# Kernel optimization log

Measured on AMD Instinct MI355X. Metric: run time of the kernel, lower is better.

Reference implementation:

```python
import jax, jax.numpy as jnp
import numpy as np

B, S, D = 8, 2048, 512
LN_EPS = 1e-5

def _layernorm(x, gamma, beta):
    mu = jnp.mean(x, axis=-1, keepdims=True)
    var = jnp.mean(jnp.square(x - mu), axis=-1, keepdims=True)
    return (x - mu) * jax.lax.rsqrt(var + LN_EPS) * gamma + beta

def setup_inputs() -> dict:
    key = jax.random.key(0)
    ks = jax.random.split(key, 10)
    s_in = 1.0 / np.sqrt(2 * D)
    s_d = 1.0 / np.sqrt(D)
    return {
        "Noise_x": jax.random.normal(ks[0], (B, S, D), jnp.float32),
        "X": jax.random.normal(ks[1], (B, S, D), jnp.float32),
        "cond": jax.random.normal(ks[2], (B, S, D), jnp.float32),
        "W_gate": jax.random.normal(ks[3], (2 * D, D), jnp.float32) * s_in,
        "b_gate": jnp.zeros((D,), jnp.float32),
        "W1": jax.random.normal(ks[4], (D, 2 * D), jnp.float32) * s_d,
        "b1": jnp.zeros((2 * D,), jnp.float32),
        "W2": jax.random.normal(ks[5], (2 * D, D), jnp.float32) * s_in,
        "b2": jnp.zeros((D,), jnp.float32),
        "g1": jnp.ones((D,), jnp.float32),
        "be1": jnp.zeros((D,), jnp.float32),
        "g2": jnp.ones((D,), jnp.float32),
        "be2": jnp.zeros((D,), jnp.float32),
    }

def reference(Noise_x, X, cond, W_gate, b_gate, W1, b1, W2, b2, g1, be1, g2, be2):
    # gated fusion of noise and condition
    combined = jnp.concatenate([Noise_x, cond], axis=-1)            # [B,S,2D]
    gate = jax.nn.sigmoid(combined @ W_gate + b_gate)               # [B,S,D]
    fused = gate * Noise_x + (1.0 - gate) * cond                    # [B,S,D]
    # hand-rolled attention: Q = fused, K = V = X
    scale = 1.0 / jnp.sqrt(jnp.asarray(D, fused.dtype))
    scores = jnp.einsum('bqd,bkd->bqk', fused, X) * scale           # [B,S,S]
    attn = jax.nn.softmax(scores, axis=-1)
    attn_out = jnp.einsum('bqk,bkd->bqd', attn, X)                  # [B,S,D]
    # residual + norm, FFN (exact GELU as in torch default), residual + norm
    q = _layernorm(fused + attn_out, g1, be1)
    ff = jax.nn.gelu(q @ W1 + b1, approximate=False) @ W2 + b2
    return _layernorm(q + ff, g2, be2)
```

## Files before the change

kernel.cpp:

```cpp
#include <hip/hip_runtime.h>
#include <math.h>

typedef unsigned short ushort_t;
typedef unsigned int uint_t;
typedef __attribute__((ext_vector_type(8))) short short8;
typedef __attribute__((ext_vector_type(4))) float floatx4;

constexpr int B = 8;
constexpr int S = 2048;
constexpr int D = 512;
constexpr int BS = B * S;
constexpr float LN_EPS = 1e-5f;
constexpr float ATTN_SCALE = 0.04419417382415922f;


__device__ __forceinline__ ushort_t f2bf(float f) {
    union { float f; uint_t u; } x; x.f = f;
    uint_t r = x.u + 0x7fffu + ((x.u >> 16) & 1u);
    return (ushort_t)(r >> 16);
}
__device__ __forceinline__ float bf2f(ushort_t h) {
    union { uint_t u; float f; } y; y.u = ((uint_t)h) << 16;
    return y.f;
}
__device__ __forceinline__ short8 pack8(float4 a, float4 b) {
    short8 p;
    p[0] = (short)f2bf(a.x); p[1] = (short)f2bf(a.y);
    p[2] = (short)f2bf(a.z); p[3] = (short)f2bf(a.w);
    p[4] = (short)f2bf(b.x); p[5] = (short)f2bf(b.y);
    p[6] = (short)f2bf(b.z); p[7] = (short)f2bf(b.w);
    return p;
}

#define SWZ_DECODE(bx, by, bz)                                                 \
    int bx, by, bz;                                                            \
    {                                                                          \
        const int gx = gridDim.x, gy = gridDim.y;                              \
        const int nwg = gx * gy * (int)gridDim.z;                              \
        const int F = blockIdx.x + gx * (blockIdx.y + gy * blockIdx.z);        \
        const int L = (F & 7) * (nwg >> 3) + (F >> 3);                         \
        bx = L % gx;                                                           \
        const int l2 = L / gx;                                                 \
        by = l2 % gy;                                                          \
        bz = l2 / gy;                                                          \
    }

__device__ __forceinline__ float blk_reduce_sum(float v, float* sm) {
#pragma unroll
    for (int o = 32; o; o >>= 1) v += __shfl_down(v, o, 64);
    __syncthreads();
    if ((threadIdx.x & 63) == 0) sm[threadIdx.x >> 6] = v;
    __syncthreads();
    return sm[0] + sm[1] + sm[2] + sm[3];
}
__device__ __forceinline__ float blk_reduce_max(float v, float* sm) {
#pragma unroll
    for (int o = 32; o; o >>= 1) v = fmaxf(v, __shfl_down(v, o, 64));
    __syncthreads();
    if ((threadIdx.x & 63) == 0) sm[threadIdx.x >> 6] = v;
    __syncthreads();
    return fmaxf(fmaxf(sm[0], sm[1]), fmaxf(sm[2], sm[3]));
}

__global__ __launch_bounds__(256) void transpose_cvt(
    const float* __restrict__ in, ushort_t* __restrict__ out, int R, int C,
    ushort_t* __restrict__ out2) {
    __shared__ float tl[32][33];
    const size_t zoff = (size_t)blockIdx.z * R * C;
    const int tx = threadIdx.x & 31, ty = threadIdx.x >> 5;
    const int c0 = blockIdx.x * 32, r0 = blockIdx.y * 32;
#pragma unroll
    for (int i = 0; i < 4; i++) {
        const float v = in[zoff + (size_t)(r0 + ty + i * 8) * C + c0 + tx];
        tl[ty + i * 8][tx] = v;
        if (out2) out2[zoff + (size_t)(r0 + ty + i * 8) * C + c0 + tx] = f2bf(v);
    }
    __syncthreads();
#pragma unroll
    for (int i = 0; i < 4; i++)
        out[zoff + (size_t)(c0 + ty + i * 8) * R + r0 + tx] = f2bf(tl[tx][ty + i * 8]);
}

#define IDX128()                                                               \
    const int t = threadIdx.x;                                                 \
    const int sr = t >> 2;                                          \
    const int sc = (t & 3) * 8;                                 \
    const int lane = t & 63, w = t >> 6;                                       \
    const int fr = lane & 15, fq = lane >> 4;

#define MFMA16(Asp, Bsp)                                                       \
    {                                                                          \
        short8 af[4], bfg[4];                                                  \
        _Pragma("unroll") for (int i = 0; i < 4; i++) {                        \
            af[i]  = *(const short8*)&(Asp)[(wm + i * 16 + fr) * 40 + fq * 8]; \
            bfg[i] = *(const short8*)&(Bsp)[(wn + i * 16 + fr) * 40 + fq * 8]; \
        }                                                                      \
        _Pragma("unroll") for (int i = 0; i < 4; i++)                          \
            _Pragma("unroll") for (int j = 0; j < 4; j++)                      \
                acc[i][j] = __builtin_amdgcn_mfma_f32_16x16x32_bf16(           \
                    af[i], bfg[j], acc[i][j], 0, 0, 0);                        \
    }

#define MFMA8(Asp, Bsp)                                                        \
    {                                                                          \
        short8 af[2], bfg[4];                                                  \
        _Pragma("unroll") for (int i = 0; i < 2; i++)                          \
            af[i]  = *(const short8*)&(Asp)[(wm + i * 16 + fr) * 40 + fq * 8]; \
        _Pragma("unroll") for (int j = 0; j < 4; j++)                          \
            bfg[j] = *(const short8*)&(Bsp)[(j * 16 + fr) * 40 + fq * 8];      \
        _Pragma("unroll") for (int i = 0; i < 2; i++)                          \
            _Pragma("unroll") for (int j = 0; j < 4; j++)                      \
                acc[i][j] = __builtin_amdgcn_mfma_f32_16x16x32_bf16(           \
                    af[i], bfg[j], acc[i][j], 0, 0, 0);                        \
    }

__global__ __launch_bounds__(256) void gate_gemm(
    const float* __restrict__ NX, const float* __restrict__ CD,
    const ushort_t* __restrict__ WgT, const float* __restrict__ bg,
    ushort_t* __restrict__ Fb) {
    __shared__ ushort_t As[2][128 * 40];
    __shared__ ushort_t Bs[2][128 * 40];
    SWZ_DECODE(bx, by, bz);
    (void)bz;
    IDX128();
    const int m0 = by * 128, n0 = bx * 128;
    const int wm = (w >> 1) * 64, wn = (w & 1) * 64;
    floatx4 acc[4][4];
#pragma unroll
    for (int i = 0; i < 4; i++)
#pragma unroll
        for (int j = 0; j < 4; j++) {
            acc[i][j][0] = 0.f; acc[i][j][1] = 0.f;
            acc[i][j][2] = 0.f; acc[i][j][3] = 0.f;
        }
    const ushort_t* Bb = WgT + (size_t)n0 * 1024;

    float4 f00, f01, f10, f11;
    int4 b0, b1;
    {
        const float* p0 = NX + (size_t)(m0 + sr) * 512 + sc;
        const float* p1 = NX + (size_t)(m0 + sr + 64) * 512 + sc;
        f00 = *(const float4*)p0;  f01 = *(const float4*)(p0 + 4);
        f10 = *(const float4*)p1;  f11 = *(const float4*)(p1 + 4);
        b0 = *(const int4*)(Bb + (size_t)sr * 1024 + sc);
        b1 = *(const int4*)(Bb + (size_t)(sr + 64) * 1024 + sc);
        *(short8*)&As[0][sr * 40 + sc] = pack8(f00, f01);
        *(short8*)&As[0][(sr + 64) * 40 + sc] = pack8(f10, f11);
        *(int4*)&Bs[0][sr * 40 + sc] = b0;
        *(int4*)&Bs[0][(sr + 64) * 40 + sc] = b1;
    }
    {
        const float* p0 = NX + (size_t)(m0 + sr) * 512 + 32 + sc;
        const float* p1 = NX + (size_t)(m0 + sr + 64) * 512 + 32 + sc;
        f00 = *(const float4*)p0;  f01 = *(const float4*)(p0 + 4);
        f10 = *(const float4*)p1;  f11 = *(const float4*)(p1 + 4);
        b0 = *(const int4*)(Bb + (size_t)sr * 1024 + 32 + sc);
        b1 = *(const int4*)(Bb + (size_t)(sr + 64) * 1024 + 32 + sc);
    }
    __syncthreads();

    int cur = 0;
    for (int k0 = 0; k0 < 1024; k0 += 32) {
        MFMA16(As[cur], Bs[cur]);
        const int kn = k0 + 32;
        if (kn < 1024) {
            *(short8*)&As[cur ^ 1][sr * 40 + sc] = pack8(f00, f01);
            *(short8*)&As[cur ^ 1][(sr + 64) * 40 + sc] = pack8(f10, f11);
            *(int4*)&Bs[cur ^ 1][sr * 40 + sc] = b0;
            *(int4*)&Bs[cur ^ 1][(sr + 64) * 40 + sc] = b1;
            const int kf = kn + 32;
            if (kf < 1024) {
                const float* Asrc = (kf < 512) ? NX : CD;
                const int kk = kf & 511;
                const float* p0 = Asrc + (size_t)(m0 + sr) * 512 + kk + sc;
                const float* p1 = Asrc + (size_t)(m0 + sr + 64) * 512 + kk + sc;
                f00 = *(const float4*)p0;  f01 = *(const float4*)(p0 + 4);
                f10 = *(const float4*)p1;  f11 = *(const float4*)(p1 + 4);
                b0 = *(const int4*)(Bb + (size_t)sr * 1024 + kf + sc);
                b1 = *(const int4*)(Bb + (size_t)(sr + 64) * 1024 + kf + sc);
            }
        }
        __syncthreads();
        cur ^= 1;
    }

#pragma unroll
    for (int i = 0; i < 4; i++) {
#pragma unroll
        for (int j = 0; j < 4; j++) {
#pragma unroll
            for (int r = 0; r < 4; r++) {
                const int m = m0 + wm + i * 16 + fq * 4 + r;
                const int n = n0 + wn + j * 16 + fr;
                const float z = acc[i][j][r] + bg[n];
                const float g = 1.f / (1.f + expf(-z));
                const size_t idx = (size_t)m * 512 + n;
                Fb[idx] = f2bf(g * NX[idx] + (1.f - g) * CD[idx]);
            }
        }
    }
}

template <int EPI>
__global__ __launch_bounds__(256) void gemm2_std(
    const ushort_t* __restrict__ A, int lda, long sAz,
    const ushort_t* __restrict__ Bt, int ldb, long sBz,
    void* __restrict__ Cv, int ldc, long sCz,
    int K, const float* __restrict__ bias, float scale, int init) {
    __shared__ ushort_t As[2][128 * 40];
    __shared__ ushort_t Bs[2][128 * 40];
    SWZ_DECODE(bx, by, bz);
    IDX128();
    const int m0 = by * 128, n0 = bx * 128;
    const int wm = (w >> 1) * 64, wn = (w & 1) * 64;
    floatx4 acc[4][4];
#pragma unroll
    for (int i = 0; i < 4; i++)
#pragma unroll
        for (int j = 0; j < 4; j++) {
            acc[i][j][0] = 0.f; acc[i][j][1] = 0.f;
            acc[i][j][2] = 0.f; acc[i][j][3] = 0.f;
        }
    const ushort_t* Ab = A + (size_t)bz * sAz + (size_t)m0 * lda;
    const ushort_t* Bb = Bt + (size_t)bz * sBz + (size_t)n0 * ldb;

    int4 a0 = *(const int4*)(Ab + (size_t)sr * lda + sc);
    int4 a1 = *(const int4*)(Ab + (size_t)(sr + 64) * lda + sc);
    int4 b0 = *(const int4*)(Bb + (size_t)sr * ldb + sc);
    int4 b1 = *(const int4*)(Bb + (size_t)(sr + 64) * ldb + sc);
    *(int4*)&As[0][sr * 40 + sc] = a0;
    *(int4*)&As[0][(sr + 64) * 40 + sc] = a1;
    *(int4*)&Bs[0][sr * 40 + sc] = b0;
    *(int4*)&Bs[0][(sr + 64) * 40 + sc] = b1;
    if (32 < K) {
        a0 = *(const int4*)(Ab + (size_t)sr * lda + 32 + sc);
        a1 = *(const int4*)(Ab + (size_t)(sr + 64) * lda + 32 + sc);
        b0 = *(const int4*)(Bb + (size_t)sr * ldb + 32 + sc);
        b1 = *(const int4*)(Bb + (size_t)(sr + 64) * ldb + 32 + sc);
    }
    __syncthreads();

    int cur = 0;
    for (int k0 = 0; k0 < K; k0 += 32) {
        MFMA16(As[cur], Bs[cur]);
        const int kn = k0 + 32;
        if (kn < K) {
            *(int4*)&As[cur ^ 1][sr * 40 + sc] = a0;
            *(int4*)&As[cur ^ 1][(sr + 64) * 40 + sc] = a1;
            *(int4*)&Bs[cur ^ 1][sr * 40 + sc] = b0;
            *(int4*)&Bs[cur ^ 1][(sr + 64) * 40 + sc] = b1;
            const int kf = kn + 32;
            if (kf < K) {
                a0 = *(const int4*)(Ab + (size_t)sr * lda + kf + sc);
                a1 = *(const int4*)(Ab + (size_t)(sr + 64) * lda + kf + sc);
                b0 = *(const int4*)(Bb + (size_t)sr * ldb + kf + sc);
                b1 = *(const int4*)(Bb + (size_t)(sr + 64) * ldb + kf + sc);
            }
        }
        __syncthreads();
        cur ^= 1;
    }

#pragma unroll
    for (int i = 0; i < 4; i++) {
#pragma unroll
        for (int j = 0; j < 4; j++) {
#pragma unroll
            for (int r = 0; r < 4; r++) {
                const int m = m0 + wm + i * 16 + fq * 4 + r;
                const int n = n0 + wn + j * 16 + fr;
                float v = acc[i][j][r];
                if (EPI == 0) {
                    ushort_t* C = (ushort_t*)Cv + (size_t)bz * sCz;
                    C[(size_t)m * ldc + n] = f2bf(v * scale);
                } else if (EPI == 1) {
                    const float x = v + bias[n];
                    const float gl = 0.5f * x * (1.f + erff(x * 0.70710678118654752f));
                    ushort_t* C = (ushort_t*)Cv;
                    C[(size_t)m * ldc + n] = f2bf(gl);
                } else {
                    float* T = (float*)Cv;
                    const size_t idx = (size_t)m * ldc + n;
                    T[idx] = T[idx] + v + (init ? bias[n] : 0.f);
                }
            }
        }
    }
}

template <int EPI>
__global__ __launch_bounds__(256) void gemm3_std(
    const ushort_t* __restrict__ A, int lda, long sAz,
    const ushort_t* __restrict__ Bt, int ldb, long sBz,
    void* __restrict__ Cv, int ldc, long sCz,
    int K, const float* __restrict__ bias, float scale, int init) {
    __shared__ ushort_t As[2][128 * 40];
    __shared__ ushort_t Bs[2][64 * 40];
    SWZ_DECODE(bx, by, bz);
    IDX128();
    const int m0 = by * 128, n0 = bx * 64;
    const int wm = w * 32;
    floatx4 acc[2][4];
#pragma unroll
    for (int i = 0; i < 2; i++)
#pragma unroll
        for (int j = 0; j < 4; j++) {
            acc[i][j][0] = 0.f; acc[i][j][1] = 0.f;
            acc[i][j][2] = 0.f; acc[i][j][3] = 0.f;
        }
    const ushort_t* Ab = A + (size_t)bz * sAz + (size_t)m0 * lda;
    const ushort_t* Bb = Bt + (size_t)bz * sBz + (size_t)n0 * ldb;

    int4 a0 = *(const int4*)(Ab + (size_t)sr * lda + sc);
    int4 a1 = *(const int4*)(Ab + (size_t)(sr + 64) * lda + sc);
    int4 b0 = *(const int4*)(Bb + (size_t)sr * ldb + sc);
    *(int4*)&As[0][sr * 40 + sc] = a0;
    *(int4*)&As[0][(sr + 64) * 40 + sc] = a1;
    *(int4*)&Bs[0][sr * 40 + sc] = b0;
    if (32 < K) {
        a0 = *(const int4*)(Ab + (size_t)sr * lda + 32 + sc);
        a1 = *(const int4*)(Ab + (size_t)(sr + 64) * lda + 32 + sc);
        b0 = *(const int4*)(Bb + (size_t)sr * ldb + 32 + sc);
    }
    __syncthreads();

    int cur = 0;
    for (int k0 = 0; k0 < K; k0 += 32) {
        MFMA8(As[cur], Bs[cur]);
        const int kn = k0 + 32;
        if (kn < K) {
            *(int4*)&As[cur ^ 1][sr * 40 + sc] = a0;
            *(int4*)&As[cur ^ 1][(sr + 64) * 40 + sc] = a1;
            *(int4*)&Bs[cur ^ 1][sr * 40 + sc] = b0;
            const int kf = kn + 32;
            if (kf < K) {
                a0 = *(const int4*)(Ab + (size_t)sr * lda + kf + sc);
                a1 = *(const int4*)(Ab + (size_t)(sr + 64) * lda + kf + sc);
                b0 = *(const int4*)(Bb + (size_t)sr * ldb + kf + sc);
            }
        }
        __syncthreads();
        cur ^= 1;
    }

#pragma unroll
    for (int i = 0; i < 2; i++) {
#pragma unroll
        for (int j = 0; j < 4; j++) {
#pragma unroll
            for (int r = 0; r < 4; r++) {
                const int m = m0 + wm + i * 16 + fq * 4 + r;
                const int n = n0 + j * 16 + fr;
                float v = acc[i][j][r];
                if (EPI == 0) {
                    ushort_t* C = (ushort_t*)Cv + (size_t)bz * sCz;
                    C[(size_t)m * ldc + n] = f2bf(v * scale);
                } else if (EPI == 1) {
                    const float x = v + bias[n];
                    const float gl = 0.5f * x * (1.f + erff(x * 0.70710678118654752f));
                    ushort_t* C = (ushort_t*)Cv;
                    C[(size_t)m * ldc + n] = f2bf(gl);
                } else {
                    float* T = (float*)Cv;
                    const size_t idx = (size_t)m * ldc + n;
                    T[idx] = T[idx] + v + (init ? bias[n] : 0.f);
                }
            }
        }
    }
}

__global__ __launch_bounds__(256) void softmax_bf16(ushort_t* __restrict__ Sc) {
    __shared__ float sm[4];
    ushort_t* row = Sc + (size_t)blockIdx.x * 2048;
    const int t = threadIdx.x;
    ushort_t raw[8];
    *(int4*)raw = *(const int4*)(row + t * 8);
    float e[8];
    float mx = -1e30f;
#pragma unroll
    for (int j = 0; j < 8; j++) { e[j] = bf2f(raw[j]); mx = fmaxf(mx, e[j]); }
    mx = blk_reduce_max(mx, sm);
    float s = 0.f;
#pragma unroll
    for (int j = 0; j < 8; j++) { e[j] = expf(e[j] - mx); s += e[j]; }
    s = blk_reduce_sum(s, sm);
    const float inv = 1.f / s;
#pragma unroll
    for (int j = 0; j < 8; j++) raw[j] = f2bf(e[j] * inv);
    *(int4*)(row + t * 8) = *(const int4*)raw;
}

__global__ __launch_bounds__(256) void ln1_kernel(
    const ushort_t* __restrict__ Fb, const ushort_t* __restrict__ Ab,
    const float* __restrict__ g1, const float* __restrict__ be1,
    float* __restrict__ qf, ushort_t* __restrict__ qb) {
    __shared__ float sm[4];
    const size_t base = (size_t)blockIdx.x * 512;
    const int t = threadIdx.x;
    const float v0 = bf2f(Fb[base + t]) + bf2f(Ab[base + t]);
    const float v1 = bf2f(Fb[base + t + 256]) + bf2f(Ab[base + t + 256]);
    const float mu = blk_reduce_sum(v0 + v1, sm) * (1.f / 512.f);
    const float d0 = v0 - mu, d1 = v1 - mu;
    const float var = blk_reduce_sum(d0 * d0 + d1 * d1, sm) * (1.f / 512.f);
    const float rs = rsqrtf(var + LN_EPS);
    const float y0 = d0 * rs * g1[t] + be1[t];
    const float y1 = d1 * rs * g1[t + 256] + be1[t + 256];
    qf[base + t] = y0;          qf[base + t + 256] = y1;
    qb[base + t] = f2bf(y0);    qb[base + t + 256] = f2bf(y1);
}

__global__ __launch_bounds__(256) void ln2_kernel(
    float* __restrict__ T, const float* __restrict__ g,
    const float* __restrict__ be) {
    __shared__ float sm[4];
    const size_t base = (size_t)blockIdx.x * 512;
    const int t = threadIdx.x;
    const float v0 = T[base + t];
    const float v1 = T[base + t + 256];
    const float mu = blk_reduce_sum(v0 + v1, sm) * (1.f / 512.f);
    const float d0 = v0 - mu, d1 = v1 - mu;
    const float var = blk_reduce_sum(d0 * d0 + d1 * d1, sm) * (1.f / 512.f);
    const float rs = rsqrtf(var + LN_EPS);
    T[base + t] = d0 * rs * g[t] + be[t];
    T[base + t + 256] = d1 * rs * g[t + 256] + be[t + 256];
}

extern "C" void kernel_launch(void* const* d_in, const int* in_sizes, int n_in,
                              void* d_out, int out_size, void* d_ws, size_t ws_size,
                              hipStream_t stream) {
    const float* NX  = (const float*)d_in[0];
    const float* X   = (const float*)d_in[1];
    const float* CD  = (const float*)d_in[2];
    const float* Wg  = (const float*)d_in[3];
    const float* bg  = (const float*)d_in[4];
    const float* W1  = (const float*)d_in[5];
    const float* b1  = (const float*)d_in[6];
    const float* W2  = (const float*)d_in[7];
    const float* b2  = (const float*)d_in[8];
    const float* g1  = (const float*)d_in[9];
    const float* be1 = (const float*)d_in[10];
    const float* g2  = (const float*)d_in[11];
    const float* be2 = (const float*)d_in[12];

    ushort_t* slot0 = (ushort_t*)d_ws;
    ushort_t* slot1 = (ushort_t*)((char*)d_ws + 16777216);
    ushort_t* slot2 = (ushort_t*)((char*)d_ws + 33554432);
    ushort_t* Xb    = slot0;
    ushort_t* attnb = slot0;
    ushort_t* hbuf  = slot0;
    ushort_t* Fb    = slot1;
    ushort_t* W1T   = slot1;
    ushort_t* W2T   = slot1 + 524288;
    ushort_t* WgT   = slot2;
    ushort_t* XbT   = slot2;
    ushort_t* qb    = slot2;
    ushort_t* Scb   = (ushort_t*)d_out;
    float*    qf    = (float*)d_out;

    transpose_cvt<<<dim3(512 / 32, 1024 / 32, 1), 256, 0, stream>>>(
        Wg, WgT, 1024, 512, nullptr);

    gate_gemm<<<dim3(4, 128), 256, 0, stream>>>(NX, CD, WgT, bg, Fb);

    transpose_cvt<<<dim3(512 / 32, 2048 / 32, 8), 256, 0, stream>>>(
        X, XbT, 2048, 512, Xb);

    for (int g = 0; g < 2; g++) {
        const size_t go = (size_t)g * 4 * S * 512;
        gemm2_std<0><<<dim3(16, 16, 4), 256, 0, stream>>>(
            Fb + go, D, (long)S * D,
            Xb + go, D, (long)S * D,
            (void*)Scb, S, (long)S * S, D, nullptr, ATTN_SCALE, 0);
        softmax_bf16<<<4 * S, 256, 0, stream>>>(Scb);
        gemm3_std<0><<<dim3(8, 16, 4), 256, 0, stream>>>(
            Scb, S, (long)S * S,
            XbT + go, S, (long)D * S,
            (void*)(attnb + go), 512, (long)S * 512, S, nullptr, 1.f, 0);
    }

    ln1_kernel<<<BS, 256, 0, stream>>>(Fb, attnb, g1, be1, qf, qb);

    transpose_cvt<<<dim3(1024 / 32, 512 / 32, 1), 256, 0, stream>>>(
        W1, W1T, 512, 1024, nullptr);
    transpose_cvt<<<dim3(512 / 32, 1024 / 32, 1), 256, 0, stream>>>(
        W2, W2T, 1024, 512, nullptr);

    for (int h = 0; h < 2; h++) {
        gemm2_std<1><<<dim3(4, 128), 256, 0, stream>>>(
            qb, 512, 0, W1T + (size_t)h * 512 * 512, 512, 0,
            (void*)hbuf, 512, 0, 512, b1 + h * 512, 1.f, 0);
        gemm2_std<2><<<dim3(4, 128), 256, 0, stream>>>(
            hbuf, 512, 0, W2T + h * 512, 1024, 0,
            (void*)qf, 512, 0, 512, b2, 1.f, h == 0 ? 1 : 0);
    }

    ln2_kernel<<<BS, 256, 0, stream>>>(qf, g2, be2);
}
```

Before: 513.5 us.

## Use 512-thread blocks with 8 waves for 128x128 GEMM tiles

The gate GEMM and the generic 128x128 GEMM kernels now run with 512 threads (8 waves) per block instead of 256. Each wave computes a 64x32 sub-tile instead of 64x64, which halves the accumulators and global-load registers per thread. Each thread now stages one A row and one B row per K step. The aim is more waves in flight to hide latency, at the cost of more LDS fragment reads per MFMA and heavier barrier synchronisation.

```diff
diff --git a/kernel.cpp b/kernel.cpp
--- a/kernel.cpp
+++ b/kernel.cpp
@@ -81,40 +81,28 @@
         out[zoff + (size_t)(c0 + ty + i * 8) * R + r0 + tx] = f2bf(tl[tx][ty + i * 8]);
 }
 
-#define IDX128()                                                               \
+#define IDX512()                                                               \
     const int t = threadIdx.x;                                                 \
-    const int sr = t >> 2;                                          \
-    const int sc = (t & 3) * 8;                                 \
-    const int lane = t & 63, w = t >> 6;                                       \
+    const int srow = t >> 2;                                       \
+    const int scol = (t & 3) * 8;                               \
+    const int lane = t & 63, w = t >> 6;                           \
+    const int wm = (w >> 2) * 64, wn = (w & 3) * 32;                           \
     const int fr = lane & 15, fq = lane >> 4;
 
-#define MFMA16(Asp, Bsp)                                                       \
+#define MFMA8W(Asp, Bsp)                                                       \
     {                                                                          \
-        short8 af[4], bfg[4];                                                  \
-        _Pragma("unroll") for (int i = 0; i < 4; i++) {                        \
+        short8 af[4], bfg[2];                                                  \
+        _Pragma("unroll") for (int i = 0; i < 4; i++)                          \
             af[i]  = *(const short8*)&(Asp)[(wm + i * 16 + fr) * 40 + fq * 8]; \
-            bfg[i] = *(const short8*)&(Bsp)[(wn + i * 16 + fr) * 40 + fq * 8]; \
-        }                                                                      \
+        _Pragma("unroll") for (int j = 0; j < 2; j++)                          \
+            bfg[j] = *(const short8*)&(Bsp)[(wn + j * 16 + fr) * 40 + fq * 8]; \
         _Pragma("unroll") for (int i = 0; i < 4; i++)                          \
-            _Pragma("unroll") for (int j = 0; j < 4; j++)                      \
+            _Pragma("unroll") for (int j = 0; j < 2; j++)                      \
                 acc[i][j] = __builtin_amdgcn_mfma_f32_16x16x32_bf16(           \
                     af[i], bfg[j], acc[i][j], 0, 0, 0);                        \
     }
 
-#define MFMA8(Asp, Bsp)                                                        \
-    {                                                                          \
-        short8 af[2], bfg[4];                                                  \
-        _Pragma("unroll") for (int i = 0; i < 2; i++)                          \
-            af[i]  = *(const short8*)&(Asp)[(wm + i * 16 + fr) * 40 + fq * 8]; \
-        _Pragma("unroll") for (int j = 0; j < 4; j++)                          \
-            bfg[j] = *(const short8*)&(Bsp)[(j * 16 + fr) * 40 + fq * 8];      \
-        _Pragma("unroll") for (int i = 0; i < 2; i++)                          \
-            _Pragma("unroll") for (int j = 0; j < 4; j++)                      \
-                acc[i][j] = __builtin_amdgcn_mfma_f32_16x16x32_bf16(           \
-                    af[i], bfg[j], acc[i][j], 0, 0, 0);                        \
-    }
-
-__global__ __launch_bounds__(256) void gate_gemm(
+__global__ __launch_bounds__(512) void gate_gemm(
     const float* __restrict__ NX, const float* __restrict__ CD,
     const ushort_t* __restrict__ WgT, const float* __restrict__ bg,
     ushort_t* __restrict__ Fb) {
@@ -122,62 +110,48 @@
     __shared__ ushort_t Bs[2][128 * 40];
     SWZ_DECODE(bx, by, bz);
     (void)bz;
-    IDX128();
+    IDX512();
     const int m0 = by * 128, n0 = bx * 128;
-    const int wm = (w >> 1) * 64, wn = (w & 1) * 64;
-    floatx4 acc[4][4];
+    floatx4 acc[4][2];
 #pragma unroll
     for (int i = 0; i < 4; i++)
 #pragma unroll
-        for (int j = 0; j < 4; j++) {
+        for (int j = 0; j < 2; j++) {
             acc[i][j][0] = 0.f; acc[i][j][1] = 0.f;
             acc[i][j][2] = 0.f; acc[i][j][3] = 0.f;
         }
     const ushort_t* Bb = WgT + (size_t)n0 * 1024;
 
-    float4 f00, f01, f10, f11;
-    int4 b0, b1;
+    float4 fa0, fa1;
+    int4 b0;
     {
-        const float* p0 = NX + (size_t)(m0 + sr) * 512 + sc;
-        const float* p1 = NX + (size_t)(m0 + sr + 64) * 512 + sc;
-        f00 = *(const float4*)p0;  f01 = *(const float4*)(p0 + 4);
-        f10 = *(const float4*)p1;  f11 = *(const float4*)(p1 + 4);
-        b0 = *(const int4*)(Bb + (size_t)sr * 1024 + sc);
-        b1 = *(const int4*)(Bb + (size_t)(sr + 64) * 1024 + sc);
-        *(short8*)&As[0][sr * 40 + sc] = pack8(f00, f01);
-        *(short8*)&As[0][(sr + 64) * 40 + sc] = pack8(f10, f11);
-        *(int4*)&Bs[0][sr * 40 + sc] = b0;
-        *(int4*)&Bs[0][(sr + 64) * 40 + sc] = b1;
+        const float* p0 = NX + (size_t)(m0 + srow) * 512 + scol;
+        fa0 = *(const float4*)p0;  fa1 = *(const float4*)(p0 + 4);
+        b0 = *(const int4*)(Bb + (size_t)srow * 1024 + scol);
+        *(short8*)&As[0][srow * 40 + scol] = pack8(fa0, fa1);
+        *(int4*)&Bs[0][srow * 40 + scol] = b0;
     }
     {
-        const float* p0 = NX + (size_t)(m0 + sr) * 512 + 32 + sc;
-        const float* p1 = NX + (size_t)(m0 + sr + 64) * 512 + 32 + sc;
-        f00 = *(const float4*)p0;  f01 = *(const float4*)(p0 + 4);
-        f10 = *(const float4*)p1;  f11 = *(const float4*)(p1 + 4);
-        b0 = *(const int4*)(Bb + (size_t)sr * 1024 + 32 + sc);
-        b1 = *(const int4*)(Bb + (size_t)(sr + 64) * 1024 + 32 + sc);
+        const float* p0 = NX + (size_t)(m0 + srow) * 512 + 32 + scol;
+        fa0 = *(const float4*)p0;  fa1 = *(const float4*)(p0 + 4);
+        b0 = *(const int4*)(Bb + (size_t)srow * 1024 + 32 + scol);
     }
     __syncthreads();
 
     int cur = 0;
     for (int k0 = 0; k0 < 1024; k0 += 32) {
-        MFMA16(As[cur], Bs[cur]);
+        MFMA8W(As[cur], Bs[cur]);
         const int kn = k0 + 32;
         if (kn < 1024) {
-            *(short8*)&As[cur ^ 1][sr * 40 + sc] = pack8(f00, f01);
-            *(short8*)&As[cur ^ 1][(sr + 64) * 40 + sc] = pack8(f10, f11);
-            *(int4*)&Bs[cur ^ 1][sr * 40 + sc] = b0;
-            *(int4*)&Bs[cur ^ 1][(sr + 64) * 40 + sc] = b1;
+            *(short8*)&As[cur ^ 1][srow * 40 + scol] = pack8(fa0, fa1);
+            *(int4*)&Bs[cur ^ 1][srow * 40 + scol] = b0;
             const int kf = kn + 32;
             if (kf < 1024) {
                 const float* Asrc = (kf < 512) ? NX : CD;
                 const int kk = kf & 511;
-                const float* p0 = Asrc + (size_t)(m0 + sr) * 512 + kk + sc;
-                const float* p1 = Asrc + (size_t)(m0 + sr + 64) * 512 + kk + sc;
-                f00 = *(const float4*)p0;  f01 = *(const float4*)(p0 + 4);
-                f10 = *(const float4*)p1;  f11 = *(const float4*)(p1 + 4);
-                b0 = *(const int4*)(Bb + (size_t)sr * 1024 + kf + sc);
-                b1 = *(const int4*)(Bb + (size_t)(sr + 64) * 1024 + kf + sc);
+                const float* p0 = Asrc + (size_t)(m0 + srow) * 512 + kk + scol;
+                fa0 = *(const float4*)p0;  fa1 = *(const float4*)(p0 + 4);
+                b0 = *(const int4*)(Bb + (size_t)srow * 1024 + kf + scol);
             }
         }
         __syncthreads();
@@ -187,7 +161,7 @@
 #pragma unroll
     for (int i = 0; i < 4; i++) {
 #pragma unroll
-        for (int j = 0; j < 4; j++) {
+        for (int j = 0; j < 2; j++) {
 #pragma unroll
             for (int r = 0; r < 4; r++) {
                 const int m = m0 + wm + i * 16 + fq * 4 + r;
@@ -202,7 +176,7 @@
 }
 
 template <int EPI>
-__global__ __launch_bounds__(256) void gemm2_std(
+__global__ __launch_bounds__(512) void gemm2_std(
     const ushort_t* __restrict__ A, int lda, long sAz,
     const ushort_t* __restrict__ Bt, int ldb, long sBz,
     void* __restrict__ Cv, int ldc, long sCz,
@@ -210,51 +184,40 @@
     __shared__ ushort_t As[2][128 * 40];
     __shared__ ushort_t Bs[2][128 * 40];
     SWZ_DECODE(bx, by, bz);
-    IDX128();
+    IDX512();
     const int m0 = by * 128, n0 = bx * 128;
-    const int wm = (w >> 1) * 64, wn = (w & 1) * 64;
-    floatx4 acc[4][4];
+    floatx4 acc[4][2];
 #pragma unroll
     for (int i = 0; i < 4; i++)
 #pragma unroll
-        for (int j = 0; j < 4; j++) {
+        for (int j = 0; j < 2; j++) {
             acc[i][j][0] = 0.f; acc[i][j][1] = 0.f;
             acc[i][j][2] = 0.f; acc[i][j][3] = 0.f;
         }
     const ushort_t* Ab = A + (size_t)bz * sAz + (size_t)m0 * lda;
     const ushort_t* Bb = Bt + (size_t)bz * sBz + (size_t)n0 * ldb;
 
-    int4 a0 = *(const int4*)(Ab + (size_t)sr * lda + sc);
-    int4 a1 = *(const int4*)(Ab + (size_t)(sr + 64) * lda + sc);
-    int4 b0 = *(const int4*)(Bb + (size_t)sr * ldb + sc);
-    int4 b1 = *(const int4*)(Bb + (size_t)(sr + 64) * ldb + sc);
-    *(int4*)&As[0][sr * 40 + sc] = a0;
-    *(int4*)&As[0][(sr + 64) * 40 + sc] = a1;
-    *(int4*)&Bs[0][sr * 40 + sc] = b0;
-    *(int4*)&Bs[0][(sr + 64) * 40 + sc] = b1;
+    int4 a0 = *(const int4*)(Ab + (size_t)srow * lda + scol);
+    int4 b0 = *(const int4*)(Bb + (size_t)srow * ldb + scol);
+    *(int4*)&As[0][srow * 40 + scol] = a0;
+    *(int4*)&Bs[0][srow * 40 + scol] = b0;
     if (32 < K) {
-        a0 = *(const int4*)(Ab + (size_t)sr * lda + 32 + sc);
-        a1 = *(const int4*)(Ab + (size_t)(sr + 64) * lda + 32 + sc);
-        b0 = *(const int4*)(Bb + (size_t)sr * ldb + 32 + sc);
-        b1 = *(const int4*)(Bb + (size_t)(sr + 64) * ldb + 32 + sc);
+        a0 = *(const int4*)(Ab + (size_t)srow * lda + 32 + scol);
+        b0 = *(const int4*)(Bb + (size_t)srow * ldb + 32 + scol);
     }
     __syncthreads();
 
     int cur = 0;
     for (int k0 = 0; k0 < K; k0 += 32) {
-        MFMA16(As[cur], Bs[cur]);
+        MFMA8W(As[cur], Bs[cur]);
         const int kn = k0 + 32;
         if (kn < K) {
-            *(int4*)&As[cur ^ 1][sr * 40 + sc] = a0;
-            *(int4*)&As[cur ^ 1][(sr + 64) * 40 + sc] = a1;
-            *(int4*)&Bs[cur ^ 1][sr * 40 + sc] = b0;
-            *(int4*)&Bs[cur ^ 1][(sr + 64) * 40 + sc] = b1;
+            *(int4*)&As[cur ^ 1][srow * 40 + scol] = a0;
+            *(int4*)&Bs[cur ^ 1][srow * 40 + scol] = b0;
             const int kf = kn + 32;
             if (kf < K) {
-                a0 = *(const int4*)(Ab + (size_t)sr * lda + kf + sc);
-                a1 = *(const int4*)(Ab + (size_t)(sr + 64) * lda + kf + sc);
-                b0 = *(const int4*)(Bb + (size_t)sr * ldb + kf + sc);
-                b1 = *(const int4*)(Bb + (size_t)(sr + 64) * ldb + kf + sc);
+                a0 = *(const int4*)(Ab + (size_t)srow * lda + kf + scol);
+                b0 = *(const int4*)(Bb + (size_t)srow * ldb + kf + scol);
             }
         }
         __syncthreads();
@@ -264,7 +227,7 @@
 #pragma unroll
     for (int i = 0; i < 4; i++) {
 #pragma unroll
-        for (int j = 0; j < 4; j++) {
+        for (int j = 0; j < 2; j++) {
 #pragma unroll
             for (int r = 0; r < 4; r++) {
                 const int m = m0 + wm + i * 16 + fq * 4 + r;
@@ -288,6 +251,26 @@
     }
 }
 
+#define IDX128()                                                               \
+    const int t = threadIdx.x;                                                 \
+    const int sr = t >> 2;                                          \
+    const int sc = (t & 3) * 8;                                 \
+    const int lane = t & 63, w = t >> 6;                                       \
+    const int fr = lane & 15, fq = lane >> 4;
+
+#define MFMA8(Asp, Bsp)                                                        \
+    {                                                                          \
+        short8 af[2], bfg[4];                                                  \
+        _Pragma("unroll") for (int i = 0; i < 2; i++)                          \
+            af[i]  = *(const short8*)&(Asp)[(wm + i * 16 + fr) * 40 + fq * 8]; \
+        _Pragma("unroll") for (int j = 0; j < 4; j++)                          \
+            bfg[j] = *(const short8*)&(Bsp)[(j * 16 + fr) * 40 + fq * 8];      \
+        _Pragma("unroll") for (int i = 0; i < 2; i++)                          \
+            _Pragma("unroll") for (int j = 0; j < 4; j++)                      \
+                acc[i][j] = __builtin_amdgcn_mfma_f32_16x16x32_bf16(           \
+                    af[i], bfg[j], acc[i][j], 0, 0, 0);                        \
+    }
+
 template <int EPI>
 __global__ __launch_bounds__(256) void gemm3_std(
     const ushort_t* __restrict__ A, int lda, long sAz,
@@ -461,14 +444,14 @@
     transpose_cvt<<<dim3(512 / 32, 1024 / 32, 1), 256, 0, stream>>>(
         Wg, WgT, 1024, 512, nullptr);
 
-    gate_gemm<<<dim3(4, 128), 256, 0, stream>>>(NX, CD, WgT, bg, Fb);
+    gate_gemm<<<dim3(4, 128), 512, 0, stream>>>(NX, CD, WgT, bg, Fb);
 
     transpose_cvt<<<dim3(512 / 32, 2048 / 32, 8), 256, 0, stream>>>(
         X, XbT, 2048, 512, Xb);
 
     for (int g = 0; g < 2; g++) {
         const size_t go = (size_t)g * 4 * S * 512;
-        gemm2_std<0><<<dim3(16, 16, 4), 256, 0, stream>>>(
+        gemm2_std<0><<<dim3(16, 16, 4), 512, 0, stream>>>(
             Fb + go, D, (long)S * D,
             Xb + go, D, (long)S * D,
             (void*)Scb, S, (long)S * S, D, nullptr, ATTN_SCALE, 0);
@@ -487,10 +470,10 @@
         W2, W2T, 1024, 512, nullptr);
 
     for (int h = 0; h < 2; h++) {
-        gemm2_std<1><<<dim3(4, 128), 256, 0, stream>>>(
+        gemm2_std<1><<<dim3(4, 128), 512, 0, stream>>>(
             qb, 512, 0, W1T + (size_t)h * 512 * 512, 512, 0,
             (void*)hbuf, 512, 0, 512, b1 + h * 512, 1.f, 0);
-        gemm2_std<2><<<dim3(4, 128), 256, 0, stream>>>(
+        gemm2_std<2><<<dim3(4, 128), 512, 0, stream>>>(
             hbuf, 512, 0, W2T + h * 512, 1024, 0,
             (void*)qf, 512, 0, 512, b2, 1.f, h == 0 ? 1 : 0);
     }
```

After: 468.7 us. -8.7%, faster.
